# Optimization experiments

Hardware: AMD Instinct MI355X
Metric: run time of the kernel (lower is better)

The kernel has to match this reference:

```python
import jax, jax.numpy as jnp
import numpy as np

EMBED_DIM = 1024
NUM_HEADS = 16
HEAD_DIM = EMBED_DIM // NUM_HEADS
FF_HIDDEN = 4096
ROPE_BASE = 10000.0


def rope(x, start_pos):
    # x: [B, H, S, hd]; interleaved pair rotation
    S, hd = x.shape[2], x.shape[3]
    freqs = 1.0 / ROPE_BASE ** (jnp.arange(0, hd, 2, dtype=jnp.float32) / hd)
    t = jnp.arange(start_pos, start_pos + S, dtype=jnp.float32)
    angles = jnp.outer(t, freqs)            # [S, hd/2]
    cos, sin = jnp.cos(angles), jnp.sin(angles)
    x_even = x[..., 0::2]
    x_odd = x[..., 1::2]
    out_even = x_even * cos - x_odd * sin
    out_odd = x_even * sin + x_odd * cos
    return jnp.stack((out_even, out_odd), axis=-1).reshape(x.shape)


def rmsnorm(x, w, eps=1e-6):
    rms = jnp.sqrt(jnp.mean(x * x, axis=-1, keepdims=True) + eps)
    return x / rms * w


def setup_inputs() -> dict:
    key = jax.random.key(0)
    ks = jax.random.split(key, 8)
    D, H = EMBED_DIM, FF_HIDDEN
    s = lambda fin: 1.0 / np.sqrt(fin)
    return {
        "x": jax.random.normal(ks[0], (2, 2048, D), dtype=jnp.float32),
        "start_pos": 0,
        "norm1_w": jnp.ones((D,), jnp.float32),
        "w_qkv": jax.random.uniform(ks[1], (3 * D, D), jnp.float32, -s(D), s(D)),
        "w_o": jax.random.uniform(ks[2], (D, D), jnp.float32, -s(D), s(D)),
        "norm2_w": jnp.ones((D,), jnp.float32),
        "w_gate": jax.random.uniform(ks[3], (H, D), jnp.float32, -s(D), s(D)),
        "w_up": jax.random.uniform(ks[4], (H, D), jnp.float32, -s(D), s(D)),
        "w_down": jax.random.uniform(ks[5], (D, H), jnp.float32, -s(H), s(H)),
    }


def attention(x, w_qkv, w_o, start_pos):
    B, S, D = x.shape
    qkv = x @ w_qkv.T                         # [B, S, 3D]
    q, k, v = jnp.split(qkv, 3, axis=-1)
    def heads(t):
        return t.reshape(B, S, NUM_HEADS, HEAD_DIM).transpose(0, 2, 1, 3)
    q, k, v = heads(q), heads(k), heads(v)    # [B, H, S, hd]
    q = rope(q, start_pos)
    k = rope(k, start_pos)
    scores = jnp.einsum('bhqd,bhkd->bhqk', q, k) / np.sqrt(HEAD_DIM)
    causal = jnp.tril(jnp.ones((S, S), dtype=bool))
    scores = jnp.where(causal, scores, -jnp.inf)
    attn = jax.nn.softmax(scores, axis=-1)
    out = jnp.einsum('bhqk,bhkd->bhqd', attn, v)
    out = out.transpose(0, 2, 1, 3).reshape(B, S, D)
    return out @ w_o.T


def ffn(x, w_gate, w_up, w_down):
    return (jax.nn.silu(x @ w_gate.T) * (x @ w_up.T)) @ w_down.T


def reference(x, start_pos, norm1_w, w_qkv, w_o, norm2_w, w_gate, w_up, w_down):
    x = x + attention(rmsnorm(x, norm1_w), w_qkv, w_o, start_pos)
    x = x + ffn(rmsnorm(x, norm2_w), w_gate, w_up, w_down)
    return x
```

## Files before the change

### kernel.cpp

```cpp
#include <hip/hip_runtime.h>
#include <math.h>

typedef __bf16 bf16_t;
typedef __bf16 bf16x2 __attribute__((ext_vector_type(2)));
typedef __bf16 bf16x4 __attribute__((ext_vector_type(4)));
typedef __bf16 bf16x8 __attribute__((ext_vector_type(8)));
typedef float f32x4 __attribute__((ext_vector_type(4)));

#define B_ 2
#define S_ 2048
#define D_ 1024
#define NH 16
#define HD 64
#define FF 4096
#define NTOK (B_*S_)

__device__ __forceinline__ f32x4 mfma16(bf16x8 a, bf16x8 b, f32x4 c) {
  return __builtin_amdgcn_mfma_f32_16x16x32_bf16(a, b, c, 0, 0, 0);
}

__device__ __forceinline__ void gld_lds16(const bf16_t* g, bf16_t* l) {
  __builtin_amdgcn_global_load_lds(
      (const __attribute__((address_space(1))) void*)g,
      (__attribute__((address_space(3))) void*)l, 16, 0, 0);
}

__global__ __launch_bounds__(256) void cvt_kernel(const float* __restrict__ in,
                                                  bf16_t* __restrict__ o, int n4) {
  int i = blockIdx.x * 256 + threadIdx.x;
  const int stride = gridDim.x * 256;
  for (; i < n4; i += stride) {
    float4 v = ((const float4*)in)[i];
    bf16x4 ov;
    ov[0] = (bf16_t)v.x; ov[1] = (bf16_t)v.y; ov[2] = (bf16_t)v.z; ov[3] = (bf16_t)v.w;
    ((bf16x4*)o)[i] = ov;
  }
}

__global__ __launch_bounds__(256) void rmsnorm_kernel(const float* __restrict__ x,
                                                      const float* __restrict__ w,
                                                      bf16_t* __restrict__ o) {
  const int row = blockIdx.x;
  const float4 v = ((const float4*)(x + (size_t)row * D_))[threadIdx.x];
  float s = v.x*v.x + v.y*v.y + v.z*v.z + v.w*v.w;
  #pragma unroll
  for (int d = 32; d; d >>= 1) s += __shfl_down(s, d);
  __shared__ float acc[4];
  if ((threadIdx.x & 63) == 0) acc[threadIdx.x >> 6] = s;
  __syncthreads();
  const float scale = rsqrtf((acc[0] + acc[1] + acc[2] + acc[3]) * (1.f / D_) + 1e-6f);
  const float4 wv = ((const float4*)w)[threadIdx.x];
  bf16x4 ov;
  ov[0] = (bf16_t)(v.x * scale * wv.x);
  ov[1] = (bf16_t)(v.y * scale * wv.y);
  ov[2] = (bf16_t)(v.z * scale * wv.z);
  ov[3] = (bf16_t)(v.w * scale * wv.w);
  ((bf16x4*)(o + (size_t)row * D_))[threadIdx.x] = ov;
}

template<int MODE>
__global__ __launch_bounds__(256) void gemm_kernel(
    const bf16_t* __restrict__ A, const bf16_t* __restrict__ W,
    int M, int N, int K,
    float* __restrict__ outF, bf16_t* __restrict__ outB,
    const float* __restrict__ res, const bf16_t* __restrict__ gate) {
  __shared__ __align__(16) bf16_t lA[128 * 32];
  __shared__ __align__(16) bf16_t lB[128 * 32];
  const int tid = threadIdx.x;
  const int wave = tid >> 6, lane = tid & 63;
  const int r = lane & 15, kg = lane >> 4;
  const int bm = blockIdx.y * 128, bn = blockIdx.x * 128;
  const int wr = (wave >> 1) * 64, wc = (wave & 1) * 64;
  const bf16_t* Ab = A + (size_t)bm * K;
  const bf16_t* Wb = W + (size_t)bn * K;

  f32x4 acc[4][4] = {};
  for (int k0 = 0; k0 < K; k0 += 32) {
    __syncthreads();
    {
      const int cb0 = (wave << 6);
      const int c0 = cb0 + lane;
      gld_lds16(Ab + (size_t)(c0 >> 2) * K + k0 + (c0 & 3) * 8, lA + cb0 * 8);
      gld_lds16(Wb + (size_t)(c0 >> 2) * K + k0 + (c0 & 3) * 8, lB + cb0 * 8);
      const int cb1 = cb0 + 256;
      const int c1 = cb1 + lane;
      gld_lds16(Ab + (size_t)(c1 >> 2) * K + k0 + (c1 & 3) * 8, lA + cb1 * 8);
      gld_lds16(Wb + (size_t)(c1 >> 2) * K + k0 + (c1 & 3) * 8, lB + cb1 * 8);
    }
    __syncthreads();
    bf16x8 af[4], bfr[4];
    #pragma unroll
    for (int m = 0; m < 4; ++m)
      af[m] = *(const bf16x8*)&lA[(wr + m * 16 + r) * 32 + kg * 8];
    #pragma unroll
    for (int n = 0; n < 4; ++n)
      bfr[n] = *(const bf16x8*)&lB[(wc + n * 16 + r) * 32 + kg * 8];
    #pragma unroll
    for (int m = 0; m < 4; ++m)
      #pragma unroll
      for (int n = 0; n < 4; ++n)
        acc[m][n] = mfma16(af[m], bfr[n], acc[m][n]);
  }
  #pragma unroll
  for (int m = 0; m < 4; ++m) {
    const int row0 = bm + wr + m * 16 + kg * 4;
    #pragma unroll
    for (int n = 0; n < 4; ++n) {
      const int col = bn + wc + n * 16 + r;
      #pragma unroll
      for (int g2 = 0; g2 < 4; ++g2) {
        const size_t idx = (size_t)(row0 + g2) * N + col;
        const float v = acc[m][n][g2];
        if (MODE == 0) {
          outB[idx] = (bf16_t)v;
        } else if (MODE == 1) {
          outF[idx] = v + res[idx];
        } else {
          const float gf = (float)gate[idx];
          outB[idx] = (bf16_t)(v * gf / (1.f + __expf(-gf)));
        }
      }
    }
  }
}

__global__ __launch_bounds__(256) void rope_kernel(const bf16_t* __restrict__ qkv,
                                                   bf16_t* __restrict__ q_r,
                                                   bf16_t* __restrict__ k_r,
                                                   const int* __restrict__ start_pos) {
  const int bs = blockIdx.x;
  const int b = bs >> 11, s = bs & (S_ - 1);
  const float t = (float)(s + start_pos[0]);
  const bf16_t* rowp = qkv + (size_t)bs * 3072;
  #pragma unroll
  for (int i = 0; i < 4; ++i) {
    const int p = threadIdx.x + 256 * i;
    const int mat = p >> 9;
    const int rem = p & 511;
    const int h = rem >> 5, d2 = rem & 31;
    const float freq = expf((float)d2 * -0.2878231366242557f);
    float sn, cs;
    sincosf(t * freq, &sn, &cs);
    const bf16x2 e2 = *(const bf16x2*)(rowp + mat * 1024 + h * 64 + 2 * d2);
    const float e = (float)e2[0], od = (float)e2[1];
    bf16x2 ov;
    ov[0] = (bf16_t)(e * cs - od * sn);
    ov[1] = (bf16_t)(e * sn + od * cs);
    bf16_t* dst = (mat ? k_r : q_r) + ((size_t)(b * NH + h) * S_ + s) * HD + 2 * d2;
    *(bf16x2*)dst = ov;
  }
}

__global__ __launch_bounds__(256) void vtrans_kernel(const bf16_t* __restrict__ qkv,
                                                     bf16_t* __restrict__ vt) {
  const int bh = blockIdx.y, b = bh >> 4, h = bh & 15;
  const int s0 = blockIdx.x * 64;
  __shared__ bf16_t tile[64][65];
  #pragma unroll
  for (int i = 0; i < 16; ++i) {
    const int idx = threadIdx.x + 256 * i;
    const int sl = idx >> 6, d = idx & 63;
    tile[sl][d] = qkv[(size_t)(b * S_ + s0 + sl) * 3072 + 2048 + h * 64 + d];
  }
  __syncthreads();
  #pragma unroll
  for (int i = 0; i < 16; ++i) {
    const int idx = threadIdx.x + 256 * i;
    const int dl = idx >> 6, sl = idx & 63;
    vt[((size_t)bh * HD + dl) * S_ + s0 + sl] = tile[sl][dl];
  }
}

__global__ __launch_bounds__(256) void attn_kernel(const bf16_t* __restrict__ qr,
                                                   const bf16_t* __restrict__ kr,
                                                   const bf16_t* __restrict__ vt,
                                                   bf16_t* __restrict__ out) {
  const int bh = blockIdx.y, b = bh >> 4, h = bh & 15;
  const int wave = threadIdx.x >> 6, lane = threadIdx.x & 63;
  const int r = lane & 15, kg = lane >> 4;
  const int qbase = blockIdx.x * 64 + wave * 16;
  const bf16_t* qp = qr + ((size_t)bh * S_ + qbase) * HD;
  const bf16x8 qf0 = *(const bf16x8*)&qp[r * HD + kg * 8];
  const bf16x8 qf1 = *(const bf16x8*)&qp[r * HD + 32 + kg * 8];
  f32x4 o[4] = {};
  float mrow[4] = {-1e30f, -1e30f, -1e30f, -1e30f};
  float lrow[4] = {0.f, 0.f, 0.f, 0.f};
  __shared__ __align__(16) bf16_t plds[4][16 * 32];
  bf16_t* pw = plds[wave];
  const bf16_t* kb_p = kr + (size_t)bh * S_ * HD;
  const bf16_t* vb_p = vt + (size_t)bh * HD * S_;
  const int limit = qbase + 16;
  for (int kb = 0; kb < limit; kb += 32) {
    f32x4 s0 = {}, s1 = {};
    const bf16_t* k0p = kb_p + (size_t)(kb + r) * HD;
    s0 = mfma16(qf0, *(const bf16x8*)&k0p[kg * 8], s0);
    s0 = mfma16(qf1, *(const bf16x8*)&k0p[32 + kg * 8], s0);
    const bf16_t* k1p = k0p + 16 * HD;
    s1 = mfma16(qf0, *(const bf16x8*)&k1p[kg * 8], s1);
    s1 = mfma16(qf1, *(const bf16x8*)&k1p[32 + kg * 8], s1);
    float alpha[4];
    #pragma unroll
    for (int g2 = 0; g2 < 4; ++g2) {
      const int qrow = qbase + kg * 4 + g2;
      const float a0 = (kb + r      <= qrow) ? s0[g2] * 0.125f : -1e30f;
      const float a1 = (kb + 16 + r <= qrow) ? s1[g2] * 0.125f : -1e30f;
      float mx = fmaxf(a0, a1);
      mx = fmaxf(mx, __shfl_xor(mx, 1));
      mx = fmaxf(mx, __shfl_xor(mx, 2));
      mx = fmaxf(mx, __shfl_xor(mx, 4));
      mx = fmaxf(mx, __shfl_xor(mx, 8));
      const float nm = fmaxf(mrow[g2], mx);
      alpha[g2] = __expf(mrow[g2] - nm);
      mrow[g2] = nm;
      const float p0 = __expf(a0 - nm);
      const float p1 = __expf(a1 - nm);
      float sm = p0 + p1;
      sm += __shfl_xor(sm, 1);
      sm += __shfl_xor(sm, 2);
      sm += __shfl_xor(sm, 4);
      sm += __shfl_xor(sm, 8);
      lrow[g2] = lrow[g2] * alpha[g2] + sm;
      pw[(kg * 4 + g2) * 32 + r] = (bf16_t)p0;
      pw[(kg * 4 + g2) * 32 + 16 + r] = (bf16_t)p1;
      o[0][g2] *= alpha[g2];
      o[1][g2] *= alpha[g2];
      o[2][g2] *= alpha[g2];
      o[3][g2] *= alpha[g2];
    }
    asm volatile("s_waitcnt lgkmcnt(0)" ::: "memory");
    const bf16x8 pf = *(const bf16x8*)&pw[r * 32 + kg * 8];
    asm volatile("s_waitcnt lgkmcnt(0)" ::: "memory");
    #pragma unroll
    for (int tt = 0; tt < 4; ++tt) {
      const bf16_t* vp = vb_p + (size_t)(tt * 16 + r) * S_ + kb + kg * 8;
      o[tt] = mfma16(pf, *(const bf16x8*)vp, o[tt]);
    }
  }
  #pragma unroll
  for (int tt = 0; tt < 4; ++tt)
    #pragma unroll
    for (int g2 = 0; g2 < 4; ++g2) {
      const int srow = qbase + kg * 4 + g2;
      out[(size_t)(b * S_ + srow) * D_ + h * HD + tt * 16 + r] =
          (bf16_t)(o[tt][g2] / lrow[g2]);
    }
}

extern "C" void kernel_launch(void* const* d_in, const int* in_sizes, int n_in,
                              void* d_out, int out_size, void* d_ws, size_t ws_size,
                              hipStream_t stream) {
  const float* x     = (const float*)d_in[0];
  const int*   sp    = (const int*)d_in[1];
  const float* n1w   = (const float*)d_in[2];
  const float* wqkv  = (const float*)d_in[3];
  const float* wo    = (const float*)d_in[4];
  const float* n2w   = (const float*)d_in[5];
  const float* wgate = (const float*)d_in[6];
  const float* wup   = (const float*)d_in[7];
  const float* wdown = (const float*)d_in[8];

  char* p = (char*)d_ws;
  bf16_t* wqkv_b = (bf16_t*)p; p += (size_t)3 * D_ * D_ * 2;
  bf16_t* wo_b   = (bf16_t*)p; p += (size_t)D_ * D_ * 2;
  bf16_t* wg_b   = (bf16_t*)p; p += (size_t)FF * D_ * 2;
  bf16_t* wu_b   = (bf16_t*)p; p += (size_t)FF * D_ * 2;
  bf16_t* wd_b   = (bf16_t*)p; p += (size_t)FF * D_ * 2;
  bf16_t* xn     = (bf16_t*)p; p += (size_t)NTOK * D_ * 2;
  float*  x1     = (float*)p;  p += (size_t)NTOK * D_ * 4;
  char* pool = p;
  bf16_t* qkv    = (bf16_t*)(pool);
  bf16_t* q_r    = (bf16_t*)(pool + (size_t)25165824);
  bf16_t* k_r    = (bf16_t*)(pool + (size_t)33554432);
  bf16_t* v_t    = (bf16_t*)(pool + (size_t)41943040);
  bf16_t* attn_o = (bf16_t*)(pool + (size_t)50331648);
  bf16_t* gbuf   = (bf16_t*)(pool);
  bf16_t* hbuf   = (bf16_t*)(pool + (size_t)33554432);

  cvt_kernel<<<dim3(1024), dim3(256), 0, stream>>>(wqkv,  wqkv_b, 3 * D_ * D_ / 4);
  cvt_kernel<<<dim3(1024), dim3(256), 0, stream>>>(wo,    wo_b,   D_ * D_ / 4);
  cvt_kernel<<<dim3(1024), dim3(256), 0, stream>>>(wgate, wg_b,   FF * D_ / 4);
  cvt_kernel<<<dim3(1024), dim3(256), 0, stream>>>(wup,   wu_b,   FF * D_ / 4);
  cvt_kernel<<<dim3(1024), dim3(256), 0, stream>>>(wdown, wd_b,   FF * D_ / 4);

  rmsnorm_kernel<<<dim3(NTOK), dim3(256), 0, stream>>>(x, n1w, xn);

  gemm_kernel<0><<<dim3(3 * D_ / 128, NTOK / 128), dim3(256), 0, stream>>>(
      xn, wqkv_b, NTOK, 3 * D_, D_, nullptr, qkv, nullptr, nullptr);

  rope_kernel<<<dim3(NTOK), dim3(256), 0, stream>>>(qkv, q_r, k_r, sp);
  vtrans_kernel<<<dim3(S_ / 64, B_ * NH), dim3(256), 0, stream>>>(qkv, v_t);

  attn_kernel<<<dim3(S_ / 64, B_ * NH), dim3(256), 0, stream>>>(q_r, k_r, v_t, attn_o);

  gemm_kernel<1><<<dim3(D_ / 128, NTOK / 128), dim3(256), 0, stream>>>(
      attn_o, wo_b, NTOK, D_, D_, x1, nullptr, x, nullptr);

  rmsnorm_kernel<<<dim3(NTOK), dim3(256), 0, stream>>>(x1, n2w, xn);

  gemm_kernel<0><<<dim3(FF / 128, NTOK / 128), dim3(256), 0, stream>>>(
      xn, wg_b, NTOK, FF, D_, nullptr, gbuf, nullptr, nullptr);

  gemm_kernel<2><<<dim3(FF / 128, NTOK / 128), dim3(256), 0, stream>>>(
      xn, wu_b, NTOK, FF, D_, nullptr, hbuf, nullptr, gbuf);

  gemm_kernel<1><<<dim3(D_ / 128, NTOK / 128), dim3(256), 0, stream>>>(
      hbuf, wd_b, NTOK, D_, FF, (float*)d_out, nullptr, x1, nullptr);
}
```

Measured before the change: 645.4 us.

## Restructure attention kernel with transposed S tiles, register P, and causal tile pairing

The attention kernel now computes S transposed (K as the A operand), so each lane holds a full query column. That keeps the row max and sum reductions to two cross-lane shuffles and lets P be packed straight into registers for the PV MFMA, with no LDS round trip. The key block grows from 32 to 64 per iteration. Each workgroup processes a pair of query tiles (i and 31-i) to balance the causal workload, and the grid is halved. RoPE frequency computation switches to exp2f. Register pressure rises from the larger tile, and the per-block serial work doubles.

```diff
diff --git a/kernel.cpp b/kernel.cpp
--- a/kernel.cpp
+++ b/kernel.cpp
@@ -138,7 +138,7 @@
     const int mat = p >> 9;
     const int rem = p & 511;
     const int h = rem >> 5, d2 = rem & 31;
-    const float freq = expf((float)d2 * -0.2878231366242557f);
+    const float freq = exp2f((float)d2 * -0.4152410118609203f);
     float sn, cs;
     sincosf(t * freq, &sn, &cs);
     const bf16x2 e2 = *(const bf16x2*)(rowp + mat * 1024 + h * 64 + 2 * d2);
@@ -178,72 +178,99 @@
   const int bh = blockIdx.y, b = bh >> 4, h = bh & 15;
   const int wave = threadIdx.x >> 6, lane = threadIdx.x & 63;
   const int r = lane & 15, kg = lane >> 4;
-  const int qbase = blockIdx.x * 64 + wave * 16;
-  const bf16_t* qp = qr + ((size_t)bh * S_ + qbase) * HD;
-  const bf16x8 qf0 = *(const bf16x8*)&qp[r * HD + kg * 8];
-  const bf16x8 qf1 = *(const bf16x8*)&qp[r * HD + 32 + kg * 8];
-  f32x4 o[4] = {};
-  float mrow[4] = {-1e30f, -1e30f, -1e30f, -1e30f};
-  float lrow[4] = {0.f, 0.f, 0.f, 0.f};
-  __shared__ __align__(16) bf16_t plds[4][16 * 32];
-  bf16_t* pw = plds[wave];
   const bf16_t* kb_p = kr + (size_t)bh * S_ * HD;
   const bf16_t* vb_p = vt + (size_t)bh * HD * S_;
-  const int limit = qbase + 16;
-  for (int kb = 0; kb < limit; kb += 32) {
-    f32x4 s0 = {}, s1 = {};
-    const bf16_t* k0p = kb_p + (size_t)(kb + r) * HD;
-    s0 = mfma16(qf0, *(const bf16x8*)&k0p[kg * 8], s0);
-    s0 = mfma16(qf1, *(const bf16x8*)&k0p[32 + kg * 8], s0);
-    const bf16_t* k1p = k0p + 16 * HD;
-    s1 = mfma16(qf0, *(const bf16x8*)&k1p[kg * 8], s1);
-    s1 = mfma16(qf1, *(const bf16x8*)&k1p[32 + kg * 8], s1);
-    float alpha[4];
-    #pragma unroll
-    for (int g2 = 0; g2 < 4; ++g2) {
-      const int qrow = qbase + kg * 4 + g2;
-      const float a0 = (kb + r      <= qrow) ? s0[g2] * 0.125f : -1e30f;
-      const float a1 = (kb + 16 + r <= qrow) ? s1[g2] * 0.125f : -1e30f;
-      float mx = fmaxf(a0, a1);
-      mx = fmaxf(mx, __shfl_xor(mx, 1));
-      mx = fmaxf(mx, __shfl_xor(mx, 2));
-      mx = fmaxf(mx, __shfl_xor(mx, 4));
-      mx = fmaxf(mx, __shfl_xor(mx, 8));
-      const float nm = fmaxf(mrow[g2], mx);
-      alpha[g2] = __expf(mrow[g2] - nm);
-      mrow[g2] = nm;
-      const float p0 = __expf(a0 - nm);
-      const float p1 = __expf(a1 - nm);
-      float sm = p0 + p1;
-      sm += __shfl_xor(sm, 1);
-      sm += __shfl_xor(sm, 2);
-      sm += __shfl_xor(sm, 4);
-      sm += __shfl_xor(sm, 8);
-      lrow[g2] = lrow[g2] * alpha[g2] + sm;
-      pw[(kg * 4 + g2) * 32 + r] = (bf16_t)p0;
-      pw[(kg * 4 + g2) * 32 + 16 + r] = (bf16_t)p1;
-      o[0][g2] *= alpha[g2];
-      o[1][g2] *= alpha[g2];
-      o[2][g2] *= alpha[g2];
-      o[3][g2] *= alpha[g2];
+
+  #pragma unroll
+  for (int ti = 0; ti < 2; ++ti) {
+    const int tile = ti ? (31 - blockIdx.x) : blockIdx.x;
+    const int qbase = tile * 64 + wave * 16;
+    const bf16_t* qp = qr + ((size_t)bh * S_ + qbase) * HD;
+    const bf16x8 qf0 = *(const bf16x8*)&qp[r * HD + kg * 8];
+    const bf16x8 qf1 = *(const bf16x8*)&qp[r * HD + 32 + kg * 8];
+    f32x4 o[4] = {};
+    float m = -1e30f, l = 0.f;
+    const int limit = qbase + 16;
+    for (int kb = 0; kb < limit; kb += 64) {
+      f32x4 st[4];
+      #pragma unroll
+      for (int f = 0; f < 4; ++f) {
+        const bf16_t* kp = kb_p + (size_t)(kb + f * 16 + r) * HD;
+        f32x4 z = {};
+        z = mfma16(*(const bf16x8*)&kp[kg * 8], qf0, z);
+        z = mfma16(*(const bf16x8*)&kp[32 + kg * 8], qf1, z);
+        st[f] = z;
+      }
+      float sc[4][4];
+      float mx = -1e30f;
+      #pragma unroll
+      for (int f = 0; f < 4; ++f)
+        #pragma unroll
+        for (int g2 = 0; g2 < 4; ++g2) {
+          const int k = kb + f * 16 + kg * 4 + g2;
+          const float v = (k <= qbase + r) ? st[f][g2] * 0.125f : -1e30f;
+          sc[f][g2] = v;
+          mx = fmaxf(mx, v);
+        }
+      mx = fmaxf(mx, __shfl_xor(mx, 16));
+      mx = fmaxf(mx, __shfl_xor(mx, 32));
+      const float nm = fmaxf(m, mx);
+      const float alpha = __expf(m - nm);
+      m = nm;
+      float psum = 0.f;
+      float pe[4][4];
+      #pragma unroll
+      for (int f = 0; f < 4; ++f)
+        #pragma unroll
+        for (int g2 = 0; g2 < 4; ++g2) {
+          const float p = __expf(sc[f][g2] - nm);
+          pe[f][g2] = p;
+          psum += p;
+        }
+      psum += __shfl_xor(psum, 16);
+      psum += __shfl_xor(psum, 32);
+      l = l * alpha + psum;
+      bf16x8 PA[2];
+      #pragma unroll
+      for (int fa = 0; fa < 2; ++fa) {
+        bf16x8 v;
+        #pragma unroll
+        for (int j = 0; j < 4; ++j) v[j] = (bf16_t)pe[2 * fa][j];
+        #pragma unroll
+        for (int j = 0; j < 4; ++j) v[4 + j] = (bf16_t)pe[2 * fa + 1][j];
+        PA[fa] = v;
+      }
+      float av[4];
+      #pragma unroll
+      for (int g2 = 0; g2 < 4; ++g2) av[g2] = __shfl(alpha, kg * 4 + g2);
+      #pragma unroll
+      for (int dblk = 0; dblk < 4; ++dblk)
+        #pragma unroll
+        for (int g2 = 0; g2 < 4; ++g2) o[dblk][g2] *= av[g2];
+      #pragma unroll
+      for (int dblk = 0; dblk < 4; ++dblk) {
+        const bf16_t* vp = vb_p + (size_t)(dblk * 16 + r) * S_ + kb;
+        #pragma unroll
+        for (int fa = 0; fa < 2; ++fa) {
+          union { bf16x8 v; bf16x4 hf[2]; } bv;
+          bv.hf[0] = *(const bf16x4*)&vp[fa * 32 + kg * 4];
+          bv.hf[1] = *(const bf16x4*)&vp[fa * 32 + 16 + kg * 4];
+          o[dblk] = mfma16(PA[fa], bv.v, o[dblk]);
+        }
+      }
     }
-    asm volatile("s_waitcnt lgkmcnt(0)" ::: "memory");
-    const bf16x8 pf = *(const bf16x8*)&pw[r * 32 + kg * 8];
-    asm volatile("s_waitcnt lgkmcnt(0)" ::: "memory");
-    #pragma unroll
-    for (int tt = 0; tt < 4; ++tt) {
-      const bf16_t* vp = vb_p + (size_t)(tt * 16 + r) * S_ + kb + kg * 8;
-      o[tt] = mfma16(pf, *(const bf16x8*)vp, o[tt]);
-    }
-  }
-  #pragma unroll
-  for (int tt = 0; tt < 4; ++tt)
-    #pragma unroll
-    for (int g2 = 0; g2 < 4; ++g2) {
-      const int srow = qbase + kg * 4 + g2;
-      out[(size_t)(b * S_ + srow) * D_ + h * HD + tt * 16 + r] =
-          (bf16_t)(o[tt][g2] / lrow[g2]);
-    }
+    float lv[4];
+    #pragma unroll
+    for (int g2 = 0; g2 < 4; ++g2) lv[g2] = __shfl(l, kg * 4 + g2);
+    #pragma unroll
+    for (int dblk = 0; dblk < 4; ++dblk)
+      #pragma unroll
+      for (int g2 = 0; g2 < 4; ++g2) {
+        const int srow = qbase + kg * 4 + g2;
+        out[(size_t)(b * S_ + srow) * D_ + h * HD + dblk * 16 + r] =
+            (bf16_t)(o[dblk][g2] / lv[g2]);
+      }
+  }
 }
 
 extern "C" void kernel_launch(void* const* d_in, const int* in_sizes, int n_in,
@@ -290,7 +317,7 @@
   rope_kernel<<<dim3(NTOK), dim3(256), 0, stream>>>(qkv, q_r, k_r, sp);
   vtrans_kernel<<<dim3(S_ / 64, B_ * NH), dim3(256), 0, stream>>>(qkv, v_t);
 
-  attn_kernel<<<dim3(S_ / 64, B_ * NH), dim3(256), 0, stream>>>(q_r, k_r, v_t, attn_o);
+  attn_kernel<<<dim3(16, B_ * NH), dim3(256), 0, stream>>>(q_r, k_r, v_t, attn_o);
 
   gemm_kernel<1><<<dim3(D_ / 128, NTOK / 128), dim3(256), 0, stream>>>(
       attn_o, wo_b, NTOK, D_, D_, x1, nullptr, x, nullptr);
```

New measurement: 622.0 us. 1.04x faster.
